# Kernel tuning notes

Hardware: AMD Instinct MI355X
Metric: run time of the kernel (lower is better)

The kernel has to match this reference:

```python
import jax, jax.numpy as jnp
import numpy as np

N = 50000   # nodes
E = 800000  # edges
G = 64      # graphs in the batch
DIN = 128
DOUT = 256


def _lin(key, fan_in, fan_out):
    s = 1.0 / np.sqrt(fan_in)
    kw, kb = jax.random.split(key)
    W = jax.random.uniform(kw, (fan_in, fan_out), jnp.float32, -s, s)
    b = jax.random.uniform(kb, (fan_out,), jnp.float32, -s, s)
    return W, b


def setup_inputs() -> dict:
    key = jax.random.key(0)
    ks = jax.random.split(key, 12)
    x = jax.random.normal(ks[0], (N, DIN), jnp.float32)
    edge_index = jax.random.randint(ks[1], (2, E), 0, N, dtype=jnp.int64)
    batch = jnp.sort(jax.random.randint(ks[2], (N,), 0, G, dtype=jnp.int64))
    W1, b1 = _lin(ks[3], DIN, 128)
    W2, b2 = _lin(ks[4], 128, 128)
    W3, b3 = _lin(ks[5], 128, 128)
    A1, ba1 = _lin(ks[6], DIN, 64)
    A2, ba2 = _lin(ks[7], 64, 32)
    A3, ba3 = _lin(ks[8], 32, 1)
    M1, bm1 = _lin(ks[9], 128, 128)
    M2, bm2 = _lin(ks[10], 128, DOUT)
    return dict(x=x, edge_index=edge_index, batch=batch,
                W1=W1, b1=b1, W2=W2, b2=b2, W3=W3, b3=b3,
                A1=A1, ba1=ba1, A2=A2, ba2=ba2, A3=A3, ba3=ba3,
                M1=M1, bm1=bm1, M2=M2, bm2=bm2)


def _gcn_norm(edge_index, n, dtype):
    # GCNConv default: add self-loops, symmetric normalization D^-1/2 (A+I) D^-1/2
    loop = jnp.arange(n, dtype=edge_index.dtype)
    src = jnp.concatenate([edge_index[0], loop])
    dst = jnp.concatenate([edge_index[1], loop])
    deg = jax.ops.segment_sum(jnp.ones_like(dst, dtype), dst, num_segments=n)
    dinv = jnp.where(deg > 0, jax.lax.rsqrt(deg), 0.0)
    return src, dst, dinv[src] * dinv[dst]


def _gcn(h, W, b, src, dst, norm, n):
    h = h @ W                                   # [N, F_out]
    msg = h[src] * norm[:, None]                # gather + scale (memory bound)
    return jax.ops.segment_sum(msg, dst, num_segments=n) + b


def _segment_softmax(w, batch, g):
    # per-graph softmax (PyG softmax): stabilize with segment max
    m = jax.ops.segment_max(w, batch, num_segments=g)
    e = jnp.exp(w - m[batch])
    s = jax.ops.segment_sum(e, batch, num_segments=g)
    return e / (s[batch] + 1e-16)


def reference(x, edge_index, batch,
              W1, b1, W2, b2, W3, b3,
              A1, ba1, A2, ba2, A3, ba3,
              M1, bm1, M2, bm2):
    n = x.shape[0]
    src, dst, norm = _gcn_norm(edge_index, n, x.dtype)
    relu = jax.nn.relu
    # feature branch
    f = relu(_gcn(x, W1, b1, src, dst, norm, n))
    f = relu(_gcn(f, W2, b2, src, dst, norm, n))
    f = relu(_gcn(f, W3, b3, src, dst, norm, n))
    # attention branch
    w = relu(_gcn(x, A1, ba1, src, dst, norm, n))
    w = relu(_gcn(w, A2, ba2, src, dst, norm, n))
    w = relu(_gcn(w, A3, ba3, src, dst, norm, n))   # [N, 1]
    w = _segment_softmax(w, batch, G)
    # attention-weighted sum pooling per graph
    pooled = jax.ops.segment_sum(f * w, batch, num_segments=G)  # [G, 128]
    # MLP([128,128,256], batch_norm=False): Linear+ReLU, plain last Linear
    out = relu(pooled @ M1 + bm1) @ M2 + bm2
    return out
```

## Files before the change

kernel.cpp:

```cpp
#include <hip/hip_runtime.h>
#include <hip/hip_fp16.h>
#include <math.h>


#define DIN 128
#define FH  128
#define DOUT 256
#define NBUK 128
#define SUBN 512
#define IMGCAP 16384
#define ECAP 16384

typedef float f4 __attribute__((ext_vector_type(4)));
typedef float f32x4 __attribute__((ext_vector_type(4)));
typedef _Float16 h8v __attribute__((ext_vector_type(8)));
typedef _Float16 h4v __attribute__((ext_vector_type(4)));


__global__ __launch_bounds__(256) void scan1_kernel(const int* __restrict__ cnt,
        int* __restrict__ bsum, float* __restrict__ dinv, int n) {
    __shared__ int sm[256];
    int tid = threadIdx.x;
    int base = blockIdx.x * 512;
    int a = (base + tid < n) ? cnt[base + tid] : 0;
    int b = (base + 256 + tid < n) ? cnt[base + 256 + tid] : 0;
    if (base + tid < n)       dinv[base + tid]       = rsqrtf((float)(a + 1));
    if (base + 256 + tid < n) dinv[base + 256 + tid] = rsqrtf((float)(b + 1));
    sm[tid] = a + b;
    __syncthreads();
    for (int off = 128; off > 0; off >>= 1) {
        if (tid < off) sm[tid] += sm[tid + off];
        __syncthreads();
    }
    if (tid == 0) bsum[blockIdx.x] = sm[0];
}

__global__ void scan2_kernel(const int* __restrict__ bsum, int* __restrict__ boff,
                             int* __restrict__ rpN, int nb) {
    if (threadIdx.x == 0) {
        int run = 0;
        for (int i = 0; i < nb; ++i) { boff[i] = run; run += bsum[i]; }
        *rpN = run;
    }
}

__global__ __launch_bounds__(256) void scan3_kernel(const int* __restrict__ cnt,
        const int* __restrict__ boff, int* __restrict__ rp, int n) {
    __shared__ int sm[256];
    int tid = threadIdx.x;
    int base = blockIdx.x * 512;
    int i0 = base + 2 * tid;
    int c0 = (i0 < n) ? cnt[i0] : 0;
    int c1 = (i0 + 1 < n) ? cnt[i0 + 1] : 0;
    int ps = c0 + c1;
    sm[tid] = ps;
    __syncthreads();
    for (int off = 1; off < 256; off <<= 1) {
        int v = (tid >= off) ? sm[tid - off] : 0;
        __syncthreads();
        sm[tid] += v;
        __syncthreads();
    }
    int excl = sm[tid] - ps + boff[blockIdx.x];
    if (i0 < n) rp[i0] = excl;
    if (i0 + 1 < n) rp[i0 + 1] = excl + c0;
}

__global__ __launch_bounds__(256) void ebucket_kernel(const int* __restrict__ src,
        const int* __restrict__ dst, int* __restrict__ bcur,
        unsigned long long* __restrict__ entries, int* __restrict__ cnt,
        int E, int shift) {
    __shared__ int lcnt[NBUK], lbase[NBUK], lcur[NBUK];
    const int tid = threadIdx.x;
    const int e0 = blockIdx.x * 2048;
    if (tid < NBUK) lcnt[tid] = 0;
    __syncthreads();
    int s_[8], d_[8];
    #pragma unroll
    for (int k = 0; k < 8; ++k) {
        int e = e0 + k * 256 + tid;
        if (e < E) {
            s_[k] = src[e];
            d_[k] = dst[e];
            atomicAdd(&lcnt[d_[k] >> shift], 1);
            atomicAdd(&cnt[d_[k]], 1);
        } else {
            d_[k] = -1;
        }
    }
    __syncthreads();
    if (tid < NBUK) {
        lbase[tid] = lcnt[tid] ? atomicAdd(&bcur[tid], lcnt[tid]) : 0;
        lcur[tid] = 0;
    }
    __syncthreads();
    #pragma unroll
    for (int k = 0; k < 8; ++k) {
        if (d_[k] >= 0) {
            int b = d_[k] >> shift;
            int idx = lbase[b] + atomicAdd(&lcur[b], 1);
            if (idx < (b + 1) * ECAP)
                entries[(size_t)idx] =
                    ((unsigned long long)(unsigned)d_[k] << 32) | (unsigned)s_[k];
        }
    }
}

__global__ __launch_bounds__(512) void ecsr_kernel(
        const unsigned long long* __restrict__ entries,
        const int* __restrict__ rp, const float* __restrict__ dinv,
        long long* __restrict__ cn, int n, int shift) {
    __shared__ long long img[IMGCAP];
    __shared__ int hist[SUBN];
    __shared__ int lcur[SUBN];
    __shared__ int sm[SUBN];
    __shared__ float dl[SUBN];
    const int b = blockIdx.x;
    const int n0 = b << shift;
    if (n0 >= n) return;
    const int n1 = min(n0 + (1 << shift), n);
    const int base = rp[n0];
    const int len  = rp[n1] - base;
    const size_t ebase = (size_t)b * ECAP;
    const int tid = threadIdx.x;
    hist[tid] = 0;
    lcur[tid] = 0;
    if (n0 + tid < n1) dl[tid] = dinv[n0 + tid];
    __syncthreads();
    for (int i = tid; i < len; i += 512)
        atomicAdd(&hist[(int)(entries[ebase + i] >> 32) - n0], 1);
    __syncthreads();
    int v = hist[tid];
    sm[tid] = v;
    __syncthreads();
    for (int off = 1; off < SUBN; off <<= 1) {
        int t = (tid >= off) ? sm[tid - off] : 0;
        __syncthreads();
        sm[tid] += t;
        __syncthreads();
    }
    hist[tid] = sm[tid] - v;
    __syncthreads();
    const bool fits = (len <= IMGCAP);
    for (int i = tid; i < len; i += 512) {
        unsigned long long e = entries[ebase + i];
        int d  = (int)(e >> 32) - n0;
        int sx = (int)(unsigned)(e & 0xffffffffu);
        int pos = hist[d] + atomicAdd(&lcur[d], 1);
        float w = dinv[sx] * dl[d];
        long long val = (long long)(unsigned)sx | ((long long)__float_as_int(w) << 32);
        if (fits) img[pos] = val;
        else      cn[base + pos] = val;
    }
    __syncthreads();
    if (fits)
        for (int i = tid; i < len; i += 512) cn[base + i] = img[i];
}

__global__ void gstart_kernel(const int* __restrict__ batch, int* __restrict__ gstart,
                              int n, int g) {
    int t = threadIdx.x;
    if (t > g) return;
    int lo = 0, hi = n;
    while (lo < hi) {
        int mid = (lo + hi) >> 1;
        if (batch[mid] < t) lo = mid + 1; else hi = mid;
    }
    gstart[t] = lo;
}

__global__ void cvt16_kernel(const float* __restrict__ in, __half* __restrict__ outh,
                             long n8) {
    long i = (long)blockIdx.x * 256 + threadIdx.x;
    if (i >= n8) return;
    f4 a = ((const f4*)in)[2 * i];
    f4 b = ((const f4*)in)[2 * i + 1];
    __half2 h0 = __float22half2_rn(make_float2(a.x, a.y));
    __half2 h1 = __float22half2_rn(make_float2(a.z, a.w));
    __half2 h2 = __float22half2_rn(make_float2(b.x, b.y));
    __half2 h3 = __float22half2_rn(make_float2(b.z, b.w));
    uint4 st;
    st.x = *(unsigned*)&h0; st.y = *(unsigned*)&h1;
    st.z = *(unsigned*)&h2; st.w = *(unsigned*)&h3;
    ((uint4*)outh)[i] = st;
}


__device__ __forceinline__ void wsplit(const float* __restrict__ W,
        _Float16* __restrict__ Th, _Float16* __restrict__ Tl,
        int fin, int fout, int i) {
    int r = i / fout, c = i % fout;
    float w = W[i];
    _Float16 h = (_Float16)w;
    Th[c * fin + r] = h;
    Tl[c * fin + r] = (_Float16)(w - (float)h);
}

__global__ __launch_bounds__(256) void wprep_kernel(const float* __restrict__ W1,
        const float* __restrict__ W2, const float* __restrict__ W3,
        const float* __restrict__ A1, const float* __restrict__ A2,
        _Float16* __restrict__ T, int* __restrict__ bcur) {
    int i = blockIdx.x * 256 + threadIdx.x;
    if (blockIdx.x == 0 && threadIdx.x < NBUK) bcur[threadIdx.x] = threadIdx.x * ECAP;
    if (i < 16384)       wsplit(W1, T,          T + 16384,  128, 128, i);
    else if (i < 32768)  wsplit(W2, T + 32768,  T + 49152,  128, 128, i - 16384);
    else if (i < 49152)  wsplit(W3, T + 65536,  T + 81920,  128, 128, i - 32768);
    else if (i < 57344)  wsplit(A1, T + 98304,  T + 106496, 128, 64,  i - 49152);
    else if (i < 59392)  wsplit(A2, T + 114688, T + 116736, 64,  32,  i - 57344);
}


__global__ __launch_bounds__(256) void fusedl1_kernel(const float* __restrict__ Y,
        const _Float16* __restrict__ T, const float* __restrict__ b1,
        const float* __restrict__ ba1, __half* __restrict__ t2,
        __half* __restrict__ u2, int n) {
    constexpr int LSTR  = 136;
    constexpr int LSTRB = 72;
    __shared__ _Float16 Yh[64 * LSTR], Yl[64 * LSTR];
    __shared__ _Float16 Fh[64 * LSTR], Fl[64 * LSTR];
    const int tid  = threadIdx.x;
    const int w    = tid >> 6;
    const int lane = tid & 63;
    const int bk   = (lane >> 4) * 8;
    const int cl   = lane & 15;
    const long row0 = (long)blockIdx.x * 64;

    for (int i = tid; i < 64 * 32; i += 256) {
        int r = i >> 5, c4 = i & 31;
        long gr = row0 + r;
        float4 v = {0.f, 0.f, 0.f, 0.f};
        if (gr < n) v = *(const float4*)&Y[gr * 128 + c4 * 4];
        _Float16 h0 = (_Float16)v.x, h1 = (_Float16)v.y;
        _Float16 h2 = (_Float16)v.z, h3 = (_Float16)v.w;
        *(h4v*)&Yh[r * LSTR + c4 * 4] = (h4v){h0, h1, h2, h3};
        *(h4v*)&Yl[r * LSTR + c4 * 4] =
            (h4v){(_Float16)(v.x - (float)h0), (_Float16)(v.y - (float)h1),
                  (_Float16)(v.z - (float)h2), (_Float16)(v.w - (float)h3)};
    }
    __syncthreads();

    {
        const _Float16* W1h = T;
        const _Float16* W1l = T + 16384;
        h8v Bh[2][4], Bl[2][4];
        #pragma unroll
        for (int ct = 0; ct < 2; ++ct) {
            int c = w * 32 + ct * 16 + cl;
            #pragma unroll
            for (int kk = 0; kk < 4; ++kk) {
                Bh[ct][kk] = *(const h8v*)&W1h[c * 128 + kk * 32 + bk];
                Bl[ct][kk] = *(const h8v*)&W1l[c * 128 + kk * 32 + bk];
            }
        }
        f32x4 acc[4][2];
        #pragma unroll
        for (int rt = 0; rt < 4; ++rt)
            #pragma unroll
            for (int ct = 0; ct < 2; ++ct) acc[rt][ct] = (f32x4){0.f,0.f,0.f,0.f};
        #pragma unroll
        for (int rt = 0; rt < 4; ++rt) {
            int r = rt * 16 + cl;
            #pragma unroll
            for (int kk = 0; kk < 4; ++kk) {
                h8v ah = *(const h8v*)&Yh[r * LSTR + kk * 32 + bk];
                h8v al = *(const h8v*)&Yl[r * LSTR + kk * 32 + bk];
                #pragma unroll
                for (int ct = 0; ct < 2; ++ct) {
                    acc[rt][ct] = __builtin_amdgcn_mfma_f32_16x16x32_f16(ah, Bh[ct][kk], acc[rt][ct], 0, 0, 0);
                    acc[rt][ct] = __builtin_amdgcn_mfma_f32_16x16x32_f16(ah, Bl[ct][kk], acc[rt][ct], 0, 0, 0);
                    acc[rt][ct] = __builtin_amdgcn_mfma_f32_16x16x32_f16(al, Bh[ct][kk], acc[rt][ct], 0, 0, 0);
                }
            }
        }
        #pragma unroll
        for (int rt = 0; rt < 4; ++rt) {
            int rowb = rt * 16 + (lane >> 4) * 4;
            #pragma unroll
            for (int ct = 0; ct < 2; ++ct) {
                int col = w * 32 + ct * 16 + cl;
                float bv = b1[col];
                #pragma unroll
                for (int j = 0; j < 4; ++j) {
                    float v = fmaxf(acc[rt][ct][j] + bv, 0.f);
                    _Float16 h = (_Float16)v;
                    Fh[(rowb + j) * LSTR + col] = h;
                    Fl[(rowb + j) * LSTR + col] = (_Float16)(v - (float)h);
                }
            }
        }
    }
    __syncthreads();

    {
        const _Float16* W2h = T + 32768;
        const _Float16* W2l = T + 49152;
        h8v Bh[2][4], Bl[2][4];
        #pragma unroll
        for (int ct = 0; ct < 2; ++ct) {
            int c = w * 32 + ct * 16 + cl;
            #pragma unroll
            for (int kk = 0; kk < 4; ++kk) {
                Bh[ct][kk] = *(const h8v*)&W2h[c * 128 + kk * 32 + bk];
                Bl[ct][kk] = *(const h8v*)&W2l[c * 128 + kk * 32 + bk];
            }
        }
        f32x4 acc[4][2];
        #pragma unroll
        for (int rt = 0; rt < 4; ++rt)
            #pragma unroll
            for (int ct = 0; ct < 2; ++ct) acc[rt][ct] = (f32x4){0.f,0.f,0.f,0.f};
        #pragma unroll
        for (int rt = 0; rt < 4; ++rt) {
            int r = rt * 16 + cl;
            #pragma unroll
            for (int kk = 0; kk < 4; ++kk) {
                h8v ah = *(const h8v*)&Fh[r * LSTR + kk * 32 + bk];
                h8v al = *(const h8v*)&Fl[r * LSTR + kk * 32 + bk];
                #pragma unroll
                for (int ct = 0; ct < 2; ++ct) {
                    acc[rt][ct] = __builtin_amdgcn_mfma_f32_16x16x32_f16(ah, Bh[ct][kk], acc[rt][ct], 0, 0, 0);
                    acc[rt][ct] = __builtin_amdgcn_mfma_f32_16x16x32_f16(ah, Bl[ct][kk], acc[rt][ct], 0, 0, 0);
                    acc[rt][ct] = __builtin_amdgcn_mfma_f32_16x16x32_f16(al, Bh[ct][kk], acc[rt][ct], 0, 0, 0);
                }
            }
        }
        __syncthreads();
        #pragma unroll
        for (int rt = 0; rt < 4; ++rt) {
            long rbase = row0 + rt * 16 + (lane >> 4) * 4;
            #pragma unroll
            for (int ct = 0; ct < 2; ++ct) {
                int col = w * 32 + ct * 16 + cl;
                #pragma unroll
                for (int j = 0; j < 4; ++j) {
                    long r = rbase + j;
                    if (r < n) t2[r * 128 + col] = __float2half(acc[rt][ct][j]);
                }
            }
        }
    }

    {
        const _Float16* A1h = T + 98304;
        const _Float16* A1l = T + 106496;
        int c = w * 16 + cl;
        h8v Bh[4], Bl[4];
        #pragma unroll
        for (int kk = 0; kk < 4; ++kk) {
            Bh[kk] = *(const h8v*)&A1h[c * 128 + kk * 32 + bk];
            Bl[kk] = *(const h8v*)&A1l[c * 128 + kk * 32 + bk];
        }
        f32x4 acc[4];
        #pragma unroll
        for (int rt = 0; rt < 4; ++rt) acc[rt] = (f32x4){0.f,0.f,0.f,0.f};
        #pragma unroll
        for (int rt = 0; rt < 4; ++rt) {
            int r = rt * 16 + cl;
            #pragma unroll
            for (int kk = 0; kk < 4; ++kk) {
                h8v ah = *(const h8v*)&Yh[r * LSTR + kk * 32 + bk];
                h8v al = *(const h8v*)&Yl[r * LSTR + kk * 32 + bk];
                acc[rt] = __builtin_amdgcn_mfma_f32_16x16x32_f16(ah, Bh[kk], acc[rt], 0, 0, 0);
                acc[rt] = __builtin_amdgcn_mfma_f32_16x16x32_f16(ah, Bl[kk], acc[rt], 0, 0, 0);
                acc[rt] = __builtin_amdgcn_mfma_f32_16x16x32_f16(al, Bh[kk], acc[rt], 0, 0, 0);
            }
        }
        float bv = ba1[c];
        #pragma unroll
        for (int rt = 0; rt < 4; ++rt) {
            int rowb = rt * 16 + (lane >> 4) * 4;
            #pragma unroll
            for (int j = 0; j < 4; ++j) {
                float v = fmaxf(acc[rt][j] + bv, 0.f);
                _Float16 h = (_Float16)v;
                Fh[(rowb + j) * LSTRB + c] = h;
                Fl[(rowb + j) * LSTRB + c] = (_Float16)(v - (float)h);
            }
        }
    }
    __syncthreads();

    if (w < 2) {
        const _Float16* A2h = T + 114688;
        const _Float16* A2l = T + 116736;
        int c = w * 16 + cl;
        h8v Bh[2], Bl[2];
        #pragma unroll
        for (int kk = 0; kk < 2; ++kk) {
            Bh[kk] = *(const h8v*)&A2h[c * 64 + kk * 32 + bk];
            Bl[kk] = *(const h8v*)&A2l[c * 64 + kk * 32 + bk];
        }
        f32x4 acc[4];
        #pragma unroll
        for (int rt = 0; rt < 4; ++rt) acc[rt] = (f32x4){0.f,0.f,0.f,0.f};
        #pragma unroll
        for (int rt = 0; rt < 4; ++rt) {
            int r = rt * 16 + cl;
            #pragma unroll
            for (int kk = 0; kk < 2; ++kk) {
                h8v ah = *(const h8v*)&Fh[r * LSTRB + kk * 32 + bk];
                h8v al = *(const h8v*)&Fl[r * LSTRB + kk * 32 + bk];
                acc[rt] = __builtin_amdgcn_mfma_f32_16x16x32_f16(ah, Bh[kk], acc[rt], 0, 0, 0);
                acc[rt] = __builtin_amdgcn_mfma_f32_16x16x32_f16(ah, Bl[kk], acc[rt], 0, 0, 0);
                acc[rt] = __builtin_amdgcn_mfma_f32_16x16x32_f16(al, Bh[kk], acc[rt], 0, 0, 0);
            }
        }
        #pragma unroll
        for (int rt = 0; rt < 4; ++rt) {
            long rbase = row0 + rt * 16 + (lane >> 4) * 4;
            #pragma unroll
            for (int j = 0; j < 4; ++j) {
                long r = rbase + j;
                if (r < n) u2[r * 32 + c] = __float2half(acc[rt][j]);
            }
        }
    }
}

template<int FIN, int FOUT, int OMODE>
__global__ __launch_bounds__(256) void mgemm_kernel(const float* __restrict__ A,
        const _Float16* __restrict__ Wh, const _Float16* __restrict__ Wl,
        const float* __restrict__ bias, void* __restrict__ Cv, int n) {
    constexpr int NWC  = (FOUT / 16 < 4) ? FOUT / 16 : 4;
    constexpr int NWR  = 4 / NWC;
    constexpr int BM   = 64 * NWR;
    constexpr int CT   = FOUT / 16 / NWC;
    constexpr int KS   = FIN / 32;
    constexpr int LSTR = FIN + 8;
    __shared__ _Float16 Ahs[BM * LSTR];
    __shared__ _Float16 Als[BM * LSTR];

    const int tid  = threadIdx.x;
    const int w    = tid >> 6;
    const int lane = tid & 63;
    const long row0 = (long)blockIdx.x * BM;

    for (int i = tid; i < BM * (FIN / 4); i += 256) {
        int r  = i / (FIN / 4);
        int c4 = i % (FIN / 4);
        long gr = row0 + r;
        float4 v = {0.f, 0.f, 0.f, 0.f};
        if (gr < n) v = *(const float4*)&A[gr * FIN + c4 * 4];
        _Float16 h0 = (_Float16)v.x, h1 = (_Float16)v.y;
        _Float16 h2 = (_Float16)v.z, h3 = (_Float16)v.w;
        h4v hh = {h0, h1, h2, h3};
        h4v ll = {(_Float16)(v.x - (float)h0), (_Float16)(v.y - (float)h1),
                  (_Float16)(v.z - (float)h2), (_Float16)(v.w - (float)h3)};
        *(h4v*)&Ahs[r * LSTR + c4 * 4] = hh;
        *(h4v*)&Als[r * LSTR + c4 * 4] = ll;
    }

    const int wc = w % NWC;
    const int wr = w / NWC;
    const int colbase = wc * CT * 16;
    const int bk = (lane >> 4) * 8;
    h8v Bh[CT][KS], Bl[CT][KS];
    #pragma unroll
    for (int ct = 0; ct < CT; ++ct) {
        int c = colbase + ct * 16 + (lane & 15);
        #pragma unroll
        for (int kk = 0; kk < KS; ++kk) {
            Bh[ct][kk] = *(const h8v*)&Wh[(size_t)c * FIN + kk * 32 + bk];
            Bl[ct][kk] = *(const h8v*)&Wl[(size_t)c * FIN + kk * 32 + bk];
        }
    }

    __syncthreads();

    f32x4 acc[4][CT];
    #pragma unroll
    for (int rt = 0; rt < 4; ++rt)
        #pragma unroll
        for (int ct = 0; ct < CT; ++ct)
            acc[rt][ct] = (f32x4){0.f, 0.f, 0.f, 0.f};

    #pragma unroll
    for (int rt = 0; rt < 4; ++rt) {
        const int r = wr * 64 + rt * 16 + (lane & 15);
        #pragma unroll
        for (int kk = 0; kk < KS; ++kk) {
            h8v ah = *(const h8v*)&Ahs[r * LSTR + kk * 32 + bk];
            h8v al = *(const h8v*)&Als[r * LSTR + kk * 32 + bk];
            #pragma unroll
            for (int ct = 0; ct < CT; ++ct) {
                acc[rt][ct] = __builtin_amdgcn_mfma_f32_16x16x32_f16(ah, Bh[ct][kk], acc[rt][ct], 0, 0, 0);
                acc[rt][ct] = __builtin_amdgcn_mfma_f32_16x16x32_f16(ah, Bl[ct][kk], acc[rt][ct], 0, 0, 0);
                acc[rt][ct] = __builtin_amdgcn_mfma_f32_16x16x32_f16(al, Bh[ct][kk], acc[rt][ct], 0, 0, 0);
            }
        }
    }

    #pragma unroll
    for (int rt = 0; rt < 4; ++rt) {
        const long rbase = row0 + wr * 64 + rt * 16 + (lane >> 4) * 4;
        #pragma unroll
        for (int ct = 0; ct < CT; ++ct) {
            const int col = colbase + ct * 16 + (lane & 15);
            if (OMODE == 1) {
                const float bv = bias[col];
                #pragma unroll
                for (int j = 0; j < 4; ++j) {
                    long r = rbase + j;
                    if (r < n)
                        ((float*)Cv)[r * FOUT + col] = fmaxf(acc[rt][ct][j] + bv, 0.f);
                }
            } else {
                #pragma unroll
                for (int j = 0; j < 4; ++j) {
                    long r = rbase + j;
                    if (r < n)
                        ((__half*)Cv)[r * FOUT + col] = __float2half(acc[rt][ct][j]);
                }
            }
        }
    }
}


__device__ __forceinline__ void hacc8(float acc[8], uint4 u, float w) {
    __half2 h; float2 f;
    h = *(__half2*)&u.x; f = __half22float2(h); acc[0] += w * f.x; acc[1] += w * f.y;
    h = *(__half2*)&u.y; f = __half22float2(h); acc[2] += w * f.x; acc[3] += w * f.y;
    h = *(__half2*)&u.z; f = __half22float2(h); acc[4] += w * f.x; acc[5] += w * f.y;
    h = *(__half2*)&u.w; f = __half22float2(h); acc[6] += w * f.x; acc[7] += w * f.y;
}

template<int F, bool BR>
__global__ __launch_bounds__(256) void aggh_kernel(const __half* __restrict__ tin,
        const float* __restrict__ bias, const float* __restrict__ dinv,
        const int* __restrict__ rp, const long long* __restrict__ cn,
        float* __restrict__ out, int n) {
    constexpr int LPR   = F / 8;
    constexpr int SLOTS = 64 / LPR;
    const int lane = threadIdx.x & 63;
    const int node = blockIdx.x * 4 + (threadIdx.x >> 6);
    if (node >= n) return;
    const int l    = lane % LPR;
    const int slot = lane / LPR;
    const uint4* base = (const uint4*)tin + l;
    const int e0 = rp[node], e1 = rp[node + 1];
    float acc[8] = {0.f, 0.f, 0.f, 0.f, 0.f, 0.f, 0.f, 0.f};
    if (slot == 0) {
        float di = dinv[node];
        uint4 u = base[(size_t)node * LPR];
        hacc8(acc, u, di * di);
    }
    int p = e0 + slot;
    for (; p + 3 * SLOTS < e1; p += 4 * SLOTS) {
        long long r0 = __builtin_nontemporal_load(cn + p);
        long long r1 = __builtin_nontemporal_load(cn + p + SLOTS);
        long long r2 = __builtin_nontemporal_load(cn + p + 2 * SLOTS);
        long long r3 = __builtin_nontemporal_load(cn + p + 3 * SLOTS);
        uint4 u0 = base[(size_t)(unsigned)r0 * LPR];
        uint4 u1 = base[(size_t)(unsigned)r1 * LPR];
        uint4 u2 = base[(size_t)(unsigned)r2 * LPR];
        uint4 u3 = base[(size_t)(unsigned)r3 * LPR];
        hacc8(acc, u0, __int_as_float((int)(r0 >> 32)));
        hacc8(acc, u1, __int_as_float((int)(r1 >> 32)));
        hacc8(acc, u2, __int_as_float((int)(r2 >> 32)));
        hacc8(acc, u3, __int_as_float((int)(r3 >> 32)));
    }
    for (; p + SLOTS < e1; p += 2 * SLOTS) {
        long long r0 = __builtin_nontemporal_load(cn + p);
        long long r1 = __builtin_nontemporal_load(cn + p + SLOTS);
        uint4 u0 = base[(size_t)(unsigned)r0 * LPR];
        uint4 u1 = base[(size_t)(unsigned)r1 * LPR];
        hacc8(acc, u0, __int_as_float((int)(r0 >> 32)));
        hacc8(acc, u1, __int_as_float((int)(r1 >> 32)));
    }
    if (p < e1) {
        long long r0 = __builtin_nontemporal_load(cn + p);
        uint4 u0 = base[(size_t)(unsigned)r0 * LPR];
        hacc8(acc, u0, __int_as_float((int)(r0 >> 32)));
    }
    #pragma unroll
    for (int off = 32; off >= LPR; off >>= 1) {
        #pragma unroll
        for (int j = 0; j < 8; ++j) acc[j] += __shfl_xor(acc[j], off);
    }
    if (slot == 0) {
        if (BR) {
            #pragma unroll
            for (int j = 0; j < 8; ++j)
                acc[j] = fmaxf(acc[j] + bias[l * 8 + j], 0.f);
        }
        f4 lo = {acc[0], acc[1], acc[2], acc[3]};
        f4 hi = {acc[4], acc[5], acc[6], acc[7]};
        float* o = out + (size_t)node * F + l * 8;
        __builtin_nontemporal_store(lo, (f4*)o);
        __builtin_nontemporal_store(hi, (f4*)(o + 4));
    }
}

__global__ __launch_bounds__(256) void aggh32a_kernel(const __half* __restrict__ tin,
        const float* __restrict__ ba2, const float* __restrict__ A3,
        const float* __restrict__ dinv, const int* __restrict__ rp,
        const long long* __restrict__ cn, float* __restrict__ wlin, int n) {
    constexpr int LPR   = 4;
    constexpr int SLOTS = 16;
    const int lane = threadIdx.x & 63;
    const int node = blockIdx.x * 4 + (threadIdx.x >> 6);
    if (node >= n) return;
    const int l    = lane % LPR;
    const int slot = lane / LPR;
    const uint4* base = (const uint4*)tin + l;
    const int e0 = rp[node], e1 = rp[node + 1];
    float acc[8] = {0.f, 0.f, 0.f, 0.f, 0.f, 0.f, 0.f, 0.f};
    if (slot == 0) {
        float di = dinv[node];
        uint4 u = base[(size_t)node * LPR];
        hacc8(acc, u, di * di);
    }
    int p = e0 + slot;
    for (; p + SLOTS < e1; p += 2 * SLOTS) {
        long long r0 = __builtin_nontemporal_load(cn + p);
        long long r1 = __builtin_nontemporal_load(cn + p + SLOTS);
        uint4 u0 = base[(size_t)(unsigned)r0 * LPR];
        uint4 u1 = base[(size_t)(unsigned)r1 * LPR];
        hacc8(acc, u0, __int_as_float((int)(r0 >> 32)));
        hacc8(acc, u1, __int_as_float((int)(r1 >> 32)));
    }
    if (p < e1) {
        long long r0 = __builtin_nontemporal_load(cn + p);
        uint4 u0 = base[(size_t)(unsigned)r0 * LPR];
        hacc8(acc, u0, __int_as_float((int)(r0 >> 32)));
    }
    #pragma unroll
    for (int off = 32; off >= LPR; off >>= 1) {
        #pragma unroll
        for (int j = 0; j < 8; ++j) acc[j] += __shfl_xor(acc[j], off);
    }
    if (slot == 0) {
        float part = 0.f;
        #pragma unroll
        for (int j = 0; j < 8; ++j)
            part += fmaxf(acc[j] + ba2[l * 8 + j], 0.f) * A3[l * 8 + j];
        part += __shfl_xor(part, 1);
        part += __shfl_xor(part, 2);
        if (l == 0) wlin[node] = part;
    }
}

__global__ void agg1_kernel(const float* __restrict__ tin, const float* __restrict__ bias,
        const float* __restrict__ dinv, const int* __restrict__ rp,
        const long long* __restrict__ cn, float* __restrict__ out, int n) {
    int i = blockIdx.x * 256 + threadIdx.x;
    if (i >= n) return;
    float di = dinv[i];
    float acc = di * di * tin[i];
    int e0 = rp[i], e1 = rp[i + 1];
    int p = e0;
    float a0 = 0.f, a1 = 0.f, a2 = 0.f, a3 = 0.f;
    for (; p + 3 < e1; p += 4) {
        long long r0 = __builtin_nontemporal_load(cn + p);
        long long r1 = __builtin_nontemporal_load(cn + p + 1);
        long long r2 = __builtin_nontemporal_load(cn + p + 2);
        long long r3 = __builtin_nontemporal_load(cn + p + 3);
        a0 += __int_as_float((int)(r0 >> 32)) * tin[(int)(unsigned)r0];
        a1 += __int_as_float((int)(r1 >> 32)) * tin[(int)(unsigned)r1];
        a2 += __int_as_float((int)(r2 >> 32)) * tin[(int)(unsigned)r2];
        a3 += __int_as_float((int)(r3 >> 32)) * tin[(int)(unsigned)r3];
    }
    for (; p < e1; ++p) {
        long long r0 = __builtin_nontemporal_load(cn + p);
        a0 += __int_as_float((int)(r0 >> 32)) * tin[(int)(unsigned)r0];
    }
    acc += a0 + a1 + a2 + a3 + bias[0];
    out[i] = acc > 0.f ? acc : 0.f;
}


__global__ __launch_bounds__(256) void smexp_kernel(const float* __restrict__ w,
        const int* __restrict__ gstart, float* __restrict__ gsum,
        float* __restrict__ e) {
    const int g = blockIdx.x;
    const int a = gstart[g], b = gstart[g + 1];
    const int tid = threadIdx.x;
    __shared__ float red[4];
    float m = 0.f;
    for (int i = a + tid; i < b; i += 256) m = fmaxf(m, w[i]);
    #pragma unroll
    for (int off = 32; off > 0; off >>= 1) m = fmaxf(m, __shfl_xor(m, off));
    if ((tid & 63) == 0) red[tid >> 6] = m;
    __syncthreads();
    m = fmaxf(fmaxf(red[0], red[1]), fmaxf(red[2], red[3]));
    float s = 0.f;
    for (int i = a + tid; i < b; i += 256) {
        float ex = expf(w[i] - m);
        e[i] = ex;
        s += ex;
    }
    #pragma unroll
    for (int off = 32; off > 0; off >>= 1) s += __shfl_xor(s, off);
    __syncthreads();
    if ((tid & 63) == 0) red[tid >> 6] = s;
    __syncthreads();
    if (tid == 0) gsum[g] = red[0] + red[1] + red[2] + red[3];
}


__global__ __launch_bounds__(128) void pool_kernel(const float* __restrict__ f3,
        const float* __restrict__ e, const float* __restrict__ gsum,
        const int* __restrict__ gstart, float* __restrict__ pooled) {
    constexpr int SPG = 64;
    const int g = blockIdx.x / SPG, s = blockIdx.x % SPG;
    const int a = gstart[g], bnd = gstart[g + 1];
    const int len = bnd - a;
    if (len <= 0) return;
    const int chunk = (len + SPG - 1) / SPG;
    const int lo = a + s * chunk;
    const int hi = min(lo + chunk, bnd);
    if (lo >= hi) return;
    const float inv = 1.f / (gsum[g] + 1e-16f);
    const int tid = threadIdx.x;
    const int lane4 = tid & 31;
    const int rs    = tid >> 5;
    f4 acc = {0.f, 0.f, 0.f, 0.f};
    for (int i = lo + rs; i < hi; i += 4) {
        float w = e[i] * inv;
        f4 v = *(const f4*)&f3[(size_t)i * FH + lane4 * 4];
        acc.x += w * v.x; acc.y += w * v.y;
        acc.z += w * v.z; acc.w += w * v.w;
    }
    acc.x += __shfl_xor(acc.x, 32);
    acc.y += __shfl_xor(acc.y, 32);
    acc.z += __shfl_xor(acc.z, 32);
    acc.w += __shfl_xor(acc.w, 32);
    __shared__ float sm[128];
    if (tid >= 64 && tid < 96) *(f4*)&sm[(tid - 64) * 4] = acc;
    __syncthreads();
    if (tid < 32) {
        f4 o = *(f4*)&sm[tid * 4];
        o.x += acc.x; o.y += acc.y; o.z += acc.z; o.w += acc.w;
        float* dst = &pooled[g * FH + tid * 4];
        atomicAdd(dst + 0, o.x);
        atomicAdd(dst + 1, o.y);
        atomicAdd(dst + 2, o.z);
        atomicAdd(dst + 3, o.w);
    }
}


__global__ __launch_bounds__(128) void mlp1_kernel(const float* __restrict__ pooled,
        const float* __restrict__ M1, const float* __restrict__ bm1,
        float* __restrict__ hidden) {
    __shared__ float pr[FH];
    int g = blockIdx.x, j = threadIdx.x;
    pr[j] = pooled[g * FH + j];
    __syncthreads();
    float acc = bm1[j];
    #pragma unroll 8
    for (int k = 0; k < FH; ++k) acc += pr[k] * M1[k * FH + j];
    hidden[g * FH + j] = acc > 0.f ? acc : 0.f;
}

__global__ __launch_bounds__(256) void mlp2_kernel(const float* __restrict__ hidden,
        const float* __restrict__ M2, const float* __restrict__ bm2,
        float* __restrict__ out) {
    __shared__ float hr[FH];
    int g = blockIdx.x, j = threadIdx.x;
    if (j < FH) hr[j] = hidden[g * FH + j];
    __syncthreads();
    float acc = bm2[j];
    #pragma unroll 8
    for (int k = 0; k < FH; ++k) acc += hr[k] * M2[k * DOUT + j];
    out[g * DOUT + j] = acc;
}


extern "C" void kernel_launch(void* const* d_in, const int* in_sizes, int n_in,
                              void* d_out, int out_size, void* d_ws, size_t ws_size,
                              hipStream_t stream) {
    const float* x   = (const float*)d_in[0];
    const int*   ei  = (const int*)d_in[1];
    const int*   batch = (const int*)d_in[2];
    const float* W1  = (const float*)d_in[3];
    const float* b1  = (const float*)d_in[4];
    const float* W2  = (const float*)d_in[5];
    const float* b2  = (const float*)d_in[6];
    const float* W3  = (const float*)d_in[7];
    const float* b3  = (const float*)d_in[8];
    const float* A1  = (const float*)d_in[9];
    const float* ba1 = (const float*)d_in[10];
    const float* A2  = (const float*)d_in[11];
    const float* ba2 = (const float*)d_in[12];
    const float* A3  = (const float*)d_in[13];
    const float* ba3 = (const float*)d_in[14];
    const float* M1  = (const float*)d_in[15];
    const float* bm1 = (const float*)d_in[16];
    const float* M2  = (const float*)d_in[17];
    const float* bm2 = (const float*)d_in[18];

    const int N = in_sizes[0] / DIN;
    const int E = in_sizes[1] / 2;
    const int G = out_size / DOUT;
    const int* src = ei;
    const int* dst = ei + E;
    float* out = (float*)d_out;

    int shift = 9;
    while (((N + (1 << shift) - 1) >> shift) > NBUK) ++shift;
    const int nbuckets = (N + (1 << shift) - 1) >> shift;

    char* p = (char*)d_ws;
    auto alloc = [&](size_t bytes) -> void* {
        void* r = (void*)p;
        p += (bytes + 255) & ~(size_t)255;
        return r;
    };
    float* dinv  = (float*)alloc((size_t)N * 4);
    int*   cnt   = (int*)alloc((size_t)N * 4);
    int*   rp    = (int*)alloc((size_t)(N + 1) * 4);
    long long* cn = (long long*)alloc((size_t)E * 8);
    float* SY    = (float*)alloc((size_t)N * FH * 4);
    float* SA    = (float*)alloc((size_t)N * FH * 4);
    __half* ST   = (__half*)alloc((size_t)N * FH * 2);
    char*  SX    = (char*)alloc((size_t)N * 256);
    __half* u2   = (__half*)alloc((size_t)N * 32 * 2);
    float* wlin  = (float*)alloc((size_t)N * 4);
    float* wact  = (float*)alloc((size_t)N * 4);
    float* ebuf  = (float*)alloc((size_t)N * 4);
    float* gsum  = (float*)alloc((size_t)G * 4);
    int*   gstart= (int*)alloc((size_t)(G + 1) * 4);
    float* pooled= (float*)alloc((size_t)G * FH * 4);
    float* hidden= (float*)alloc((size_t)G * FH * 4);
    int*   bsum  = (int*)alloc(256 * 4);
    int*   boff  = (int*)alloc(256 * 4);
    int*   bcur  = (int*)alloc(NBUK * 4);
    _Float16* WT = (_Float16*)alloc((size_t)118784 * 2);

    __half* xh = (__half*)SX;
    unsigned long long* entries = (unsigned long long*)SA;

    hipMemsetAsync(cnt, 0, (size_t)N * 4, stream);
    hipMemsetAsync(pooled, 0, (size_t)G * FH * 4, stream);

    const int nb = (N + 255) / 256;
    const int NB = (N + 511) / 512;

    wprep_kernel<<<232, 256, 0, stream>>>(W1, W2, W3, A1, A2, WT, bcur);
    ebucket_kernel<<<(E + 2047) / 2048, 256, 0, stream>>>(src, dst, bcur, entries, cnt, E, shift);
    scan1_kernel<<<NB, 256, 0, stream>>>(cnt, bsum, dinv, N);
    scan2_kernel<<<1, 64, 0, stream>>>(bsum, boff, rp + N, NB);
    scan3_kernel<<<NB, 256, 0, stream>>>(cnt, boff, rp, N);
    gstart_kernel<<<1, 128, 0, stream>>>(batch, gstart, N, G);
    ecsr_kernel<<<nbuckets, 512, 0, stream>>>(entries, rp, dinv, cn, N, shift);

    const long n8 = (long)N * FH / 8;
    cvt16_kernel<<<(int)((n8 + 255) / 256), 256, 0, stream>>>(x, xh, n8);

    const int gb64 = (N + 63) / 64;
    const int agb  = (N + 3) / 4;

    aggh_kernel<FH, false><<<agb, 256, 0, stream>>>(xh, nullptr, dinv, rp, cn, SY, N);

    fusedl1_kernel<<<gb64, 256, 0, stream>>>(SY, WT, b1, ba1, (__half*)ST, u2, N);

    aggh_kernel<FH, true><<<agb, 256, 0, stream>>>(ST, b2, dinv, rp, cn, SA, N);
    mgemm_kernel<FH, FH, 2><<<gb64, 256, 0, stream>>>(SA, WT + 65536, WT + 81920, nullptr, ST, N);
    aggh_kernel<FH, true><<<agb, 256, 0, stream>>>(ST, b3, dinv, rp, cn, SY, N);

    aggh32a_kernel<<<agb, 256, 0, stream>>>(u2, ba2, A3, dinv, rp, cn, wlin, N);
    agg1_kernel<<<nb, 256, 0, stream>>>(wlin, ba3, dinv, rp, cn, wact, N);

    smexp_kernel<<<G, 256, 0, stream>>>(wact, gstart, gsum, ebuf);
    pool_kernel<<<G * 64, 128, 0, stream>>>(SY, ebuf, gsum, gstart, pooled);

    mlp1_kernel<<<G, 128, 0, stream>>>(pooled, M1, bm1, hidden);
    mlp2_kernel<<<G, 256, 0, stream>>>(hidden, M2, bm2, out);
}
```

Before: 332.7 us.

## Stage bucketed edges in LDS and count degrees per bucket with shared histograms

```diff
diff --git a/kernel.cpp b/kernel.cpp
--- a/kernel.cpp
+++ b/kernel.cpp
@@ -68,12 +68,12 @@
 
 __global__ __launch_bounds__(256) void ebucket_kernel(const int* __restrict__ src,
         const int* __restrict__ dst, int* __restrict__ bcur,
-        unsigned long long* __restrict__ entries, int* __restrict__ cnt,
-        int E, int shift) {
-    __shared__ int lcnt[NBUK], lbase[NBUK], lcur[NBUK];
+        unsigned long long* __restrict__ entries, int E, int shift) {
+    __shared__ int lcnt[NBUK], lscan[NBUK], lbase[NBUK], lcur[NBUK];
+    __shared__ unsigned long long stage[2048];
     const int tid = threadIdx.x;
     const int e0 = blockIdx.x * 2048;
-    if (tid < NBUK) lcnt[tid] = 0;
+    if (tid < NBUK) { lcnt[tid] = 0; lcur[tid] = 0; }
     __syncthreads();
     int s_[8], d_[8];
     #pragma unroll
@@ -83,27 +83,64 @@
             s_[k] = src[e];
             d_[k] = dst[e];
             atomicAdd(&lcnt[d_[k] >> shift], 1);
-            atomicAdd(&cnt[d_[k]], 1);
         } else {
             d_[k] = -1;
         }
     }
     __syncthreads();
+    if (tid < NBUK) lscan[tid] = lcnt[tid];
+    __syncthreads();
+    for (int off = 1; off < NBUK; off <<= 1) {
+        int v = 0;
+        if (tid < NBUK && tid >= off) v = lscan[tid - off];
+        __syncthreads();
+        if (tid < NBUK) lscan[tid] += v;
+        __syncthreads();
+    }
     if (tid < NBUK) {
+        lscan[tid] -= lcnt[tid];
         lbase[tid] = lcnt[tid] ? atomicAdd(&bcur[tid], lcnt[tid]) : 0;
-        lcur[tid] = 0;
     }
     __syncthreads();
     #pragma unroll
     for (int k = 0; k < 8; ++k) {
         if (d_[k] >= 0) {
             int b = d_[k] >> shift;
-            int idx = lbase[b] + atomicAdd(&lcur[b], 1);
-            if (idx < (b + 1) * ECAP)
-                entries[(size_t)idx] =
-                    ((unsigned long long)(unsigned)d_[k] << 32) | (unsigned)s_[k];
-        }
-    }
+            int pos = lscan[b] + atomicAdd(&lcur[b], 1);
+            stage[pos] = ((unsigned long long)(unsigned)d_[k] << 32) | (unsigned)s_[k];
+        }
+    }
+    __syncthreads();
+    const int total = min(2048, E - e0);
+    for (int i = tid; i < total; i += 256) {
+        int lo = 0, hi = NBUK - 1;
+        while (lo < hi) {
+            int mid = (lo + hi + 1) >> 1;
+            if (lscan[mid] <= i) lo = mid; else hi = mid - 1;
+        }
+        int idx = lbase[lo] + (i - lscan[lo]);
+        if (idx < (lo + 1) * ECAP)
+            entries[(size_t)idx] = stage[i];
+    }
+}
+
+__global__ __launch_bounds__(512) void ecount_kernel(
+        const unsigned long long* __restrict__ entries,
+        const int* __restrict__ bcur, int* __restrict__ cnt, int n, int shift) {
+    __shared__ int hist[SUBN];
+    const int b = blockIdx.x;
+    const int n0 = b << shift;
+    if (n0 >= n) return;
+    const int n1 = min(n0 + SUBN, n);
+    const int tid = threadIdx.x;
+    hist[tid] = 0;
+    __syncthreads();
+    const size_t ebase = (size_t)b * ECAP;
+    const int len = min(bcur[b] - b * ECAP, ECAP);
+    for (int i = tid; i < len; i += 512)
+        atomicAdd(&hist[(int)(entries[ebase + i] >> 32) - n0], 1);
+    __syncthreads();
+    if (n0 + tid < n1) cnt[n0 + tid] = hist[tid];
 }
 
 __global__ __launch_bounds__(512) void ecsr_kernel(
@@ -832,14 +869,14 @@
     __half* xh = (__half*)SX;
     unsigned long long* entries = (unsigned long long*)SA;
 
-    hipMemsetAsync(cnt, 0, (size_t)N * 4, stream);
     hipMemsetAsync(pooled, 0, (size_t)G * FH * 4, stream);
 
     const int nb = (N + 255) / 256;
     const int NB = (N + 511) / 512;
 
     wprep_kernel<<<232, 256, 0, stream>>>(W1, W2, W3, A1, A2, WT, bcur);
-    ebucket_kernel<<<(E + 2047) / 2048, 256, 0, stream>>>(src, dst, bcur, entries, cnt, E, shift);
+    ebucket_kernel<<<(E + 2047) / 2048, 256, 0, stream>>>(src, dst, bcur, entries, E, shift);
+    ecount_kernel<<<nbuckets, 512, 0, stream>>>(entries, bcur, cnt, N, shift);
     scan1_kernel<<<NB, 256, 0, stream>>>(cnt, bsum, dinv, N);
     scan2_kernel<<<1, 64, 0, stream>>>(bsum, boff, rp + N, NB);
     scan3_kernel<<<NB, 256, 0, stream>>>(cnt, boff, rp, N);
```

Result: faster. 309.9 us (-6.8%).
